# Performance work log

Measured on AMD Instinct MI355X. Metric: run time of the kernel, lower is better.

Reference implementation:

```python
import jax, jax.numpy as jnp
import numpy as np

KH, KW = 3, 3
K = KH * KW
PAD, STRIDE, DIL = 1, 1, 1


def _conv(x, w, b):
    y = jax.lax.conv_general_dilated(
        x, w, (STRIDE, STRIDE), ((PAD, PAD), (PAD, PAD)),
        rhs_dilation=(DIL, DIL), dimension_numbers=('NCHW', 'OIHW', 'NCHW'))
    return y + b[None, :, None, None]


def _bilinear_gather(x, py, px):
    # x: [B,C,H,W]; py, px: float sample coords [B,K,Ho,Wo]. Zero outside bounds.
    B, C, H, W = x.shape
    y0 = jnp.floor(py)
    x0 = jnp.floor(px)
    wy1 = py - y0
    wx1 = px - x0
    wy0 = 1.0 - wy1
    wx0 = 1.0 - wx1
    xf = x.reshape(B, C, H * W)

    def g(yi, xi):
        valid = (yi >= 0) & (yi < H) & (xi >= 0) & (xi < W)
        yc = jnp.clip(yi, 0, H - 1).astype(jnp.int32)
        xc = jnp.clip(xi, 0, W - 1).astype(jnp.int32)
        idx = (yc * W + xc).reshape(B, -1)                      # [B, K*Ho*Wo]
        v = jax.vmap(lambda im, ix: im[:, ix])(xf, idx)         # [B, C, K*Ho*Wo]
        v = v.reshape(B, C, *yi.shape[1:])                      # [B,C,K,Ho,Wo]
        return v * valid[:, None].astype(x.dtype)

    return ((wy0 * wx0)[:, None] * g(y0, x0)
            + (wy0 * wx1)[:, None] * g(y0, x0 + 1)
            + (wy1 * wx0)[:, None] * g(y0 + 1, x0)
            + (wy1 * wx1)[:, None] * g(y0 + 1, x0 + 1))


def setup_inputs() -> dict:
    key = jax.random.key(0)
    k1, k2, k3 = jax.random.split(key, 3)
    B, C, H, W = 8, 256, 64, 64
    x = jax.random.normal(k1, (B, C, H, W), dtype=jnp.float32)
    # small init for offset/mask conv so predicted offsets stay modest (as in DCNv2 practice)
    w_om = jax.random.normal(k2, (3 * K, C, KH, KW), dtype=jnp.float32) * 0.01
    b_om = jnp.zeros((3 * K,), dtype=jnp.float32)
    w_dc = jax.random.normal(k3, (C, C, KH, KW), dtype=jnp.float32) * (1.0 / np.sqrt(C * K))
    b_dc = jnp.zeros((C,), dtype=jnp.float32)
    return {"x": x, "w_om": w_om, "b_om": b_om, "w_dc": w_dc, "b_dc": b_dc}


def reference(x, w_om, b_om, w_dc, b_dc):
    B, C, H, W = x.shape
    om = _conv(x, w_om, b_om)                      # [B, 3K, H, W]
    offset = om[:, :2 * K].reshape(B, K, 2, H, W)  # per-tap (dy, dx)
    mask = jax.nn.sigmoid(om[:, 2 * K:])           # [B, K, H, W]
    dy, dx = offset[:, :, 0], offset[:, :, 1]
    kh = jnp.repeat(jnp.arange(KH), KW)            # [K] kernel row index
    kw = jnp.tile(jnp.arange(KW), KH)              # [K] kernel col index
    ho = jnp.arange(H)
    wo = jnp.arange(W)
    py = ho[None, None, :, None] * STRIDE - PAD + kh[None, :, None, None] * DIL + dy
    px = wo[None, None, None, :] * STRIDE - PAD + kw[None, :, None, None] * DIL + dx
    sampled = _bilinear_gather(x, py, px)          # [B,C,K,H,W]
    sampled = sampled * mask[:, None]              # modulated (DCNv2)
    w = w_dc.reshape(w_dc.shape[0], C, K)
    out = jnp.einsum('bckhw,ock->bohw', sampled, w) + b_dc[None, :, None, None]
    return out
```

## Files before the change

### kernel.cpp

```cpp
#include <hip/hip_runtime.h>
#include <hip/hip_bf16.h>
#include <hip/hip_fp16.h>
#include <math.h>

#define BB   8
#define CIN  256
#define HH   64
#define WW   64
#define OMC  27
#define HW   (HH*WW)
#define KTOT (CIN*9)
#define NPIX 32
#define SPITCH 296
#define XP1    40
#define TPW    17

typedef short bf16x8 __attribute__((ext_vector_type(8)));
typedef float f32x4  __attribute__((ext_vector_type(4)));

__device__ __forceinline__ unsigned short f2bf(float f) {
    union { float f; unsigned int u; } v; v.f = f;
    unsigned int r = v.u + 0x7FFFu + ((v.u >> 16) & 1u);
    return (unsigned short)(r >> 16);
}
__device__ __forceinline__ float bflo(unsigned int a) {
    union { unsigned int u; float f; } c; c.u = a << 16; return c.f;
}
__device__ __forceinline__ float bfhi(unsigned int a) {
    union { unsigned int u; float f; } c; c.u = a & 0xFFFF0000u; return c.f;
}

__global__ __launch_bounds__(256) void wprep_kernel(
    const float* __restrict__ w_dc, unsigned short* __restrict__ wA)
{
    int e = blockIdx.x * 256 + threadIdx.x;
    int o = e / KTOT;
    int k = e - o * KTOT;
    int c   = k / 9;
    int tap = k - c * 9;
    int kp  = (c >> 5) * 288 + tap * 32 + (c & 31);
    wA[((size_t)(kp >> 3) * 256 + o) * 8 + (kp & 7)] = f2bf(w_dc[e]);
}

__global__ __launch_bounds__(256) void womprep_kernel(
    const float* __restrict__ w_om, unsigned short* __restrict__ wOmA)
{
    int e = blockIdx.x * 256 + threadIdx.x;
    int j  = e & 7;
    int t1 = e >> 3;
    int o  = t1 & 31;
    int t2 = t1 >> 5;
    int cb = t2 & 3;
    int t3 = t2 >> 2;
    int cc = t3 & 7;
    int tap = t3 >> 3;
    int c = cc * 32 + cb * 8 + j;
    float v = (o < OMC) ? w_om[(size_t)o * KTOT + c * 9 + tap] : 0.f;
    wOmA[e] = f2bf(v);
}

__global__ __launch_bounds__(256) void om_init_kernel(
    const float* __restrict__ b_om, float* __restrict__ om)
{
    int e = blockIdx.x * 256 + threadIdx.x;
    om[e] = b_om[(e / HW) % OMC];
}

__global__ __launch_bounds__(512, 4) void om_mfma_kernel(
    const float* __restrict__ x, const unsigned short* __restrict__ wOmA,
    float* __restrict__ om)
{
    const int rawb = blockIdx.x;
    const int obid = ((rawb & 7) << 8) | (rawb >> 3);
    const int b    = obid >> 8;
    const int h    = (obid >> 2) & 63;
    const int w0   = ((obid >> 1) & 1) * 32;
    const int ksp  = obid & 1;
    const int t    = threadIdx.x;
    const int wv   = t >> 6;
    const int lane = t & 63;
    const int lq   = lane >> 4;
    const int lm   = lane & 15;
    const int mfp  = (wv >> 1) & 1;
    const int nfp  = wv & 1;
    const int p    = nfp * 16 + lm;

    __shared__ __align__(16) unsigned short sX[2 * 102 * XP1];

    unsigned short* bufA = sX;
    unsigned short* bufB = sX + 102 * XP1;

    const size_t xb_base = (size_t)b * CIN * HW;
    const float* gx_base = x + xb_base;
    const bf16x8* wOmV = reinterpret_cast<const bf16x8*>(wOmA);

    f32x4 accOm = (f32x4)(0.f);

    auto stage1 = [&](int cc, unsigned short* dst) {
        const float* gch = gx_base + (size_t)cc * 32 * HW;
#pragma unroll
        for (int i = 0; i < 7; ++i) {
            int e = t + i * 512;
            if (e < 102 * 32) {
                int cl  = e / 102;
                int rc  = e - cl * 102;
                int row = rc / 34;
                int col = rc - row * 34;
                int gy  = h - 1 + row;
                int gxx = w0 - 1 + col;
                float v = 0.f;
                if (gy >= 0 && gy < HH && (unsigned)gxx < WW)
                    v = gch[cl * HW + gy * WW + gxx];
                dst[rc * XP1 + cl] = f2bf(v);
            }
        }
    };

    stage1(ksp * 4, bufA);
    __syncthreads();
    for (int q = 0; q < 4; ++q) {
        const int ch = ksp * 4 + q;
        unsigned short* cur = (q & 1) ? bufB : bufA;
        unsigned short* nxt = (q & 1) ? bufA : bufB;
        if (q < 3) stage1(ch + 1, nxt);
#pragma unroll
        for (int tap = 0; tap < 9; ++tap) {
            int th = tap / 3, tw = tap % 3;
            bf16x8 bfr = *reinterpret_cast<const bf16x8*>(
                &cur[(th * 34 + p + tw) * XP1 + lq * 8]);
            bf16x8 af = wOmV[(((tap * 8 + ch) * 4 + lq) * 32) + mfp * 16 + lm];
            accOm = __builtin_amdgcn_mfma_f32_16x16x32_bf16(af, bfr, accOm, 0, 0, 0);
        }
        __syncthreads();
    }

    if (wv < 4) {
#pragma unroll
        for (int r = 0; r < 4; ++r) {
            int o = mfp * 16 + lq * 4 + r;
            if (o < OMC)
                atomicAdd(&om[((size_t)(b * OMC + o) * HH + h) * WW + w0 + p],
                          accOm[r]);
        }
    }
}

__global__ __launch_bounds__(512, 4) void deform_mfma_kernel(
    const float* __restrict__ x, const float* __restrict__ om,
    const unsigned short* __restrict__ wA, const float* __restrict__ b_dc,
    float* __restrict__ out)
{
    const int rawb = blockIdx.x;
    const int obid = ((rawb & 7) << 7) | (rawb >> 3);
    const int b    = obid >> 7;
    const int h    = (obid >> 1) & 63;
    const int w0   = (obid & 1) * NPIX;
    const int t    = threadIdx.x;
    const int wv   = t >> 6;
    const int lane = t & 63;
    const int lq   = lane >> 4;
    const int lm   = lane & 15;

    __shared__ __align__(16) unsigned short sS[NPIX * SPITCH];
    __shared__ __align__(16) unsigned short sR[8224];
    __shared__ __align__(16) int4 s_par[9 * NPIX];

    const size_t xb_base = (size_t)b * CIN * HW;
    const float* gx_base = x + xb_base;

    int stg[7];
#pragma unroll
    for (int i = 0; i < 7; ++i) {
        int n = t + i * 512;
        if (n < 3200) {
            int slot = n / 200;
            int rc   = n - slot * 200;
            int r    = rc / 40;
            int c    = rc - r * 40;
            int gy   = min(max(h - 2 + r, 0), HH - 1);
            int gx   = min(max(w0 - 4 + c, 0), WW - 1);
            stg[i] = (rc * TPW + slot) | (slot << 12) | ((gy * WW + gx) << 16);
        } else stg[i] = -1;
    }

    unsigned int* tWw = reinterpret_cast<unsigned int*>(sR);
    const unsigned int* tW = tWw;

    float L0[7], L1[7];
    {
        const float* gch = gx_base;
#pragma unroll
        for (int i = 0; i < 7; ++i)
            if (stg[i] >= 0) {
                int sl = (stg[i] >> 12) & 0xF;
                int go = (stg[i] >> 16) & 0xFFF;
                L0[i] = gch[(size_t)(2 * sl) * HW + go];
                L1[i] = gch[(size_t)(2 * sl + 1) * HW + go];
            }
    }

    for (int i = t; i < 712; i += 512) tWw[3400 + i] = 0u;

    if (t < 9 * NPIX) {
        int tap = t >> 5;
        int pix = t & 31;
        const float* omb = om + ((size_t)b * OMC * HH + h) * WW + w0 + pix;
        float dy = omb[(size_t)(2 * tap) * HW];
        float dx = omb[(size_t)(2 * tap + 1) * HW];
        float mv = omb[(size_t)(18 + tap) * HW];
        float m  = 1.f / (1.f + expf(-mv));
        float py = (float)(h - 1 + tap / 3) + dy;
        float px = (float)(w0 + pix - 1 + tap % 3) + dx;
        float y0f = floorf(py), x0f = floorf(px);
        float wy1 = py - y0f, wx1 = px - x0f;
        float wy0 = 1.f - wy1, wx0 = 1.f - wx1;
        int y0 = (int)y0f, x0 = (int)x0f;
        int y1 = y0 + 1, x1 = x0 + 1;
        bool yv0 = (y0 >= 0) && (y0 < HH);
        bool yv1 = (y1 >= 0) && (y1 < HH);
        bool xv0 = (x0 >= 0) && (x0 < WW);
        bool xv1 = (x1 >= 0) && (x1 < WW);
        int yc0 = min(max(y0, 0), HH - 1), yc1 = min(max(y1, 0), HH - 1);
        int xc0 = min(max(x0, 0), WW - 1), xc1 = min(max(x1, 0), WW - 1);
        float wwx = (yv0 && xv0) ? wy0 * wx0 * m : 0.f;
        float wwy = (yv0 && xv1) ? wy0 * wx1 * m : 0.f;
        float wwz = (yv1 && xv0) ? wy1 * wx0 * m : 0.f;
        float www = (yv1 && xv1) ? wy1 * wx1 * m : 0.f;
        if (xc1 == xc0) { wwx += wwy; wwy = 0.f; wwz += www; www = 0.f; }
        if (yc1 == yc0) { wwx += wwz; wwz = 0.f; wwy += www; www = 0.f; }
        bool inT = (yc0 >= h - 2) && (yc1 <= h + 2) &&
                   (xc0 >= w0 - 4) && (xc1 <= w0 + 35);
        int lb = (yc0 - (h - 2)) * 40 + (xc0 - (w0 - 4));
        int pk = (lb & 0xFF) | ((xc1 - xc0) << 8) | ((yc1 - yc0) << 9)
               | ((yc0 * WW + xc0) << 10);
        if (!inT) pk |= (int)0x80000000;
        __half2 wab = __floats2half2_rn(wwx, wwy);
        __half2 wcd = __floats2half2_rn(wwz, www);
        s_par[t] = make_int4(pk,
                             *reinterpret_cast<int*>(&wab),
                             *reinterpret_cast<int*>(&wcd), 0);
    }
    {
#pragma unroll
        for (int i = 0; i < 7; ++i)
            if (stg[i] >= 0)
                tWw[stg[i] & 0xFFF] =
                    f2bf(L0[i]) | ((unsigned int)f2bf(L1[i]) << 16);
    }
    __syncthreads();

    f32x4 acc[2][2];
#pragma unroll
    for (int i = 0; i < 2; ++i)
#pragma unroll
        for (int j = 0; j < 2; ++j)
            acc[i][j] = (f32x4)(0.f);

    const int pix  = t >> 4;
    const int slot = t & 15;

    for (int ch = 0; ch < 8; ++ch) {
#pragma unroll 3
        for (int tap = 0; tap < 9; ++tap) {
            int idx = tap * NPIX + pix;
            int4 pv = s_par[idx];
            int pk  = pv.x;
            float2 wab = __half22float2(*reinterpret_cast<__half2*>(&pv.y));
            float2 wcd = __half22float2(*reinterpret_cast<__half2*>(&pv.z));
            float v0, v1;
            if (pk >= 0) {
                int base = (pk & 0xFF) * TPW + slot;
                unsigned int a00 = tW[base];
                unsigned int a01 = tW[base + TPW];
                unsigned int a10 = tW[base + 40 * TPW];
                unsigned int a11 = tW[base + 41 * TPW];
                v0 = wab.x * bflo(a00) + wab.y * bflo(a01)
                   + wcd.x * bflo(a10) + wcd.y * bflo(a11);
                v1 = wab.x * bfhi(a00) + wab.y * bfhi(a01)
                   + wcd.x * bfhi(a10) + wcd.y * bfhi(a11);
            } else {
                int off00 = (pk >> 10) & 0xFFF;
                int d01 = (pk >> 8) & 1;
                int d10 = ((pk >> 9) & 1) * WW;
                const float* xc = x + xb_base + (size_t)(ch * 32 + 2 * slot) * HW;
                v0 = wab.x * xc[off00]       + wab.y * xc[off00 + d01]
                   + wcd.x * xc[off00 + d10] + wcd.y * xc[off00 + d10 + d01];
                xc += HW;
                v1 = wab.x * xc[off00]       + wab.y * xc[off00 + d01]
                   + wcd.x * xc[off00 + d10] + wcd.y * xc[off00 + d10 + d01];
            }
            *reinterpret_cast<unsigned int*>(
                &sS[pix * SPITCH + tap * 32 + 2 * slot]) =
                f2bf(v0) | ((unsigned int)f2bf(v1) << 16);
        }
        __syncthreads();

        if (ch < 7) {
            const float* gch = gx_base + (size_t)(ch + 1) * 32 * HW;
#pragma unroll
            for (int i = 0; i < 7; ++i)
                if (stg[i] >= 0) {
                    int sl = (stg[i] >> 12) & 0xF;
                    int go = (stg[i] >> 16) & 0xFFF;
                    L0[i] = gch[(size_t)(2 * sl) * HW + go];
                    L1[i] = gch[(size_t)(2 * sl + 1) * HW + go];
                }
        }

        const int kb_base = ch * 36;
        const bf16x8* wAv = reinterpret_cast<const bf16x8*>(wA);
#pragma unroll 1
        for (int ks = 0; ks < 9; ++ks) {
            bf16x8 bfr[2];
#pragma unroll
            for (int nf = 0; nf < 2; ++nf)
                bfr[nf] = *reinterpret_cast<const bf16x8*>(
                    &sS[(nf * 16 + lm) * SPITCH + ks * 32 + lq * 8]);
#pragma unroll
            for (int mf = 0; mf < 2; ++mf) {
                int o  = wv * 32 + mf * 16 + lm;
                int kb = kb_base + ks * 4 + lq;
                bf16x8 af = wAv[(size_t)kb * 256 + o];
#pragma unroll
                for (int nf = 0; nf < 2; ++nf)
                    acc[mf][nf] = __builtin_amdgcn_mfma_f32_16x16x32_bf16(
                        af, bfr[nf], acc[mf][nf], 0, 0, 0);
            }
        }

        if (ch < 7) {
#pragma unroll
            for (int i = 0; i < 7; ++i)
                if (stg[i] >= 0)
                    tWw[stg[i] & 0xFFF] =
                        f2bf(L0[i]) | ((unsigned int)f2bf(L1[i]) << 16);
        }
        __syncthreads();
    }

#pragma unroll
    for (int mf = 0; mf < 2; ++mf) {
#pragma unroll
        for (int r = 0; r < 4; ++r) {
            int o = wv * 32 + mf * 16 + lq * 4 + r;
            float bo = b_dc[o];
#pragma unroll
            for (int nf = 0; nf < 2; ++nf) {
                int p = nf * 16 + lm;
                out[((size_t)(b * 256 + o)) * HW + h * WW + w0 + p] = acc[mf][nf][r] + bo;
            }
        }
    }
}

extern "C" void kernel_launch(void* const* d_in, const int* in_sizes, int n_in,
                              void* d_out, int out_size, void* d_ws, size_t ws_size,
                              hipStream_t stream) {
    const float* x    = (const float*)d_in[0];
    const float* w_om = (const float*)d_in[1];
    const float* b_om = (const float*)d_in[2];
    const float* w_dc = (const float*)d_in[3];
    const float* b_dc = (const float*)d_in[4];
    float* out = (float*)d_out;

    unsigned short* wA   = (unsigned short*)d_ws;
    unsigned short* wOmA = (unsigned short*)((char*)d_ws + 1179648);
    float*          om   = (float*)((char*)d_ws + 1327104);

    wprep_kernel<<<(256 * KTOT) / 256, 256, 0, stream>>>(w_dc, wA);
    womprep_kernel<<<73728 / 256, 256, 0, stream>>>(w_om, wOmA);
    om_init_kernel<<<(BB * OMC * HW) / 256, 256, 0, stream>>>(b_om, om);
    om_mfma_kernel<<<BB * HH * 4, 512, 0, stream>>>(x, wOmA, om);
    deform_mfma_kernel<<<BB * HH * 2, 512, 0, stream>>>(x, om, wA, b_dc, out);
}
```

Baseline: 165.3 us.

## Merge weight prep kernels, drop om split-K atomics, use packed bf16 convert

Merges the two weight-prep kernels into one launch. The offset-conv kernel no longer splits the channel reduction across two blocks with atomics; each block loops over all 8 channel chunks and writes the result plus bias directly, so the om_init kernel goes away. The manual bf16 packing is replaced by the packed __float22bfloat162_rn conversion. This cuts launches, atomics and the init pass, but halves the number of om blocks and doubles each block's serial work.

```diff
diff --git a/kernel.cpp b/kernel.cpp
--- a/kernel.cpp
+++ b/kernel.cpp
@@ -23,6 +23,11 @@
     unsigned int r = v.u + 0x7FFFu + ((v.u >> 16) & 1u);
     return (unsigned short)(r >> 16);
 }
+__device__ __forceinline__ unsigned int pk2bf(float a, float b) {
+    union { __hip_bfloat162 h; unsigned int u; } c;
+    c.h = __float22bfloat162_rn(make_float2(a, b));
+    return c.u;
+}
 __device__ __forceinline__ float bflo(unsigned int a) {
     union { unsigned int u; float f; } c; c.u = a << 16; return c.f;
 }
@@ -30,52 +35,44 @@
     union { unsigned int u; float f; } c; c.u = a & 0xFFFF0000u; return c.f;
 }
 
-__global__ __launch_bounds__(256) void wprep_kernel(
-    const float* __restrict__ w_dc, unsigned short* __restrict__ wA)
+__global__ __launch_bounds__(256) void prep_kernel(
+    const float* __restrict__ w_dc, const float* __restrict__ w_om,
+    unsigned short* __restrict__ wA, unsigned short* __restrict__ wOmA)
 {
-    int e = blockIdx.x * 256 + threadIdx.x;
-    int o = e / KTOT;
-    int k = e - o * KTOT;
-    int c   = k / 9;
-    int tap = k - c * 9;
-    int kp  = (c >> 5) * 288 + tap * 32 + (c & 31);
-    wA[((size_t)(kp >> 3) * 256 + o) * 8 + (kp & 7)] = f2bf(w_dc[e]);
-}
-
-__global__ __launch_bounds__(256) void womprep_kernel(
-    const float* __restrict__ w_om, unsigned short* __restrict__ wOmA)
-{
-    int e = blockIdx.x * 256 + threadIdx.x;
-    int j  = e & 7;
-    int t1 = e >> 3;
-    int o  = t1 & 31;
-    int t2 = t1 >> 5;
-    int cb = t2 & 3;
-    int t3 = t2 >> 2;
-    int cc = t3 & 7;
-    int tap = t3 >> 3;
-    int c = cc * 32 + cb * 8 + j;
-    float v = (o < OMC) ? w_om[(size_t)o * KTOT + c * 9 + tap] : 0.f;
-    wOmA[e] = f2bf(v);
-}
-
-__global__ __launch_bounds__(256) void om_init_kernel(
+    int bid = blockIdx.x;
+    if (bid < 2304) {
+        int e = bid * 256 + threadIdx.x;
+        int o = e / KTOT;
+        int k = e - o * KTOT;
+        int c   = k / 9;
+        int tap = k - c * 9;
+        int kp  = (c >> 5) * 288 + tap * 32 + (c & 31);
+        wA[((size_t)(kp >> 3) * 256 + o) * 8 + (kp & 7)] = f2bf(w_dc[e]);
+    } else {
+        int e = (bid - 2304) * 256 + threadIdx.x;
+        int j  = e & 7;
+        int t1 = e >> 3;
+        int o  = t1 & 31;
+        int t2 = t1 >> 5;
+        int cb = t2 & 3;
+        int t3 = t2 >> 2;
+        int cc = t3 & 7;
+        int tap = t3 >> 3;
+        int c = cc * 32 + cb * 8 + j;
+        float v = (o < OMC) ? w_om[(size_t)o * KTOT + c * 9 + tap] : 0.f;
+        wOmA[e] = f2bf(v);
+    }
+}
+
+__global__ __launch_bounds__(512, 4) void om_mfma_kernel(
+    const float* __restrict__ x, const unsigned short* __restrict__ wOmA,
     const float* __restrict__ b_om, float* __restrict__ om)
 {
-    int e = blockIdx.x * 256 + threadIdx.x;
-    om[e] = b_om[(e / HW) % OMC];
-}
-
-__global__ __launch_bounds__(512, 4) void om_mfma_kernel(
-    const float* __restrict__ x, const unsigned short* __restrict__ wOmA,
-    float* __restrict__ om)
-{
     const int rawb = blockIdx.x;
-    const int obid = ((rawb & 7) << 8) | (rawb >> 3);
-    const int b    = obid >> 8;
-    const int h    = (obid >> 2) & 63;
-    const int w0   = ((obid >> 1) & 1) * 32;
-    const int ksp  = obid & 1;
+    const int obid = ((rawb & 7) << 7) | (rawb >> 3);
+    const int b    = obid >> 7;
+    const int h    = (obid >> 1) & 63;
+    const int w0   = (obid & 1) * 32;
     const int t    = threadIdx.x;
     const int wv   = t >> 6;
     const int lane = t & 63;
@@ -116,13 +113,12 @@
         }
     };
 
-    stage1(ksp * 4, bufA);
+    stage1(0, bufA);
     __syncthreads();
-    for (int q = 0; q < 4; ++q) {
-        const int ch = ksp * 4 + q;
-        unsigned short* cur = (q & 1) ? bufB : bufA;
-        unsigned short* nxt = (q & 1) ? bufA : bufB;
-        if (q < 3) stage1(ch + 1, nxt);
+    for (int ch = 0; ch < 8; ++ch) {
+        unsigned short* cur = (ch & 1) ? bufB : bufA;
+        unsigned short* nxt = (ch & 1) ? bufA : bufB;
+        if (ch < 7) stage1(ch + 1, nxt);
 #pragma unroll
         for (int tap = 0; tap < 9; ++tap) {
             int th = tap / 3, tw = tap % 3;
@@ -139,8 +135,8 @@
         for (int r = 0; r < 4; ++r) {
             int o = mfp * 16 + lq * 4 + r;
             if (o < OMC)
-                atomicAdd(&om[((size_t)(b * OMC + o) * HH + h) * WW + w0 + p],
-                          accOm[r]);
+                om[((size_t)(b * OMC + o) * HH + h) * WW + w0 + p] =
+                    accOm[r] + b_om[o];
         }
     }
 }
@@ -244,8 +240,7 @@
 #pragma unroll
         for (int i = 0; i < 7; ++i)
             if (stg[i] >= 0)
-                tWw[stg[i] & 0xFFF] =
-                    f2bf(L0[i]) | ((unsigned int)f2bf(L1[i]) << 16);
+                tWw[stg[i] & 0xFFF] = pk2bf(L0[i], L1[i]);
     }
     __syncthreads();
 
@@ -290,8 +285,7 @@
                    + wcd.x * xc[off00 + d10] + wcd.y * xc[off00 + d10 + d01];
             }
             *reinterpret_cast<unsigned int*>(
-                &sS[pix * SPITCH + tap * 32 + 2 * slot]) =
-                f2bf(v0) | ((unsigned int)f2bf(v1) << 16);
+                &sS[pix * SPITCH + tap * 32 + 2 * slot]) = pk2bf(v0, v1);
         }
         __syncthreads();
 
@@ -332,8 +326,7 @@
 #pragma unroll
             for (int i = 0; i < 7; ++i)
                 if (stg[i] >= 0)
-                    tWw[stg[i] & 0xFFF] =
-                        f2bf(L0[i]) | ((unsigned int)f2bf(L1[i]) << 16);
+                    tWw[stg[i] & 0xFFF] = pk2bf(L0[i], L1[i]);
         }
         __syncthreads();
     }
@@ -367,9 +360,7 @@
     unsigned short* wOmA = (unsigned short*)((char*)d_ws + 1179648);
     float*          om   = (float*)((char*)d_ws + 1327104);
 
-    wprep_kernel<<<(256 * KTOT) / 256, 256, 0, stream>>>(w_dc, wA);
-    womprep_kernel<<<73728 / 256, 256, 0, stream>>>(w_om, wOmA);
-    om_init_kernel<<<(BB * OMC * HW) / 256, 256, 0, stream>>>(b_om, om);
-    om_mfma_kernel<<<BB * HH * 4, 512, 0, stream>>>(x, wOmA, om);
+    prep_kernel<<<2304 + 288, 256, 0, stream>>>(w_dc, w_om, wA, wOmA);
+    om_mfma_kernel<<<BB * HH * 2, 512, 0, stream>>>(x, wOmA, b_om, om);
     deform_mfma_kernel<<<BB * HH * 2, 512, 0, stream>>>(x, om, wA, b_dc, out);
 }
```

After: 153.1 us. 7.3% less time.
